# Kernel optimization log

Measured on AMD Instinct MI355X. Metric: run time of the kernel, lower is better.

The kernel has to match this reference:

```python
import jax, jax.numpy as jnp
import numpy as np
import math

B, T, D = 2, 2048, 2048
H, KV, HD = 16, 4, 128  # n_heads, n_kv_heads, head_dim
ROPE_BASE = 10000.0


def setup_inputs() -> dict:
    key = jax.random.key(0)
    ks = jax.random.split(key, 5)
    s = 0.02
    return {
        "x": jax.random.normal(ks[0], (B, T, D), dtype=jnp.float32),
        "Wq": jax.random.normal(ks[1], (D, H * HD), dtype=jnp.float32) * s,
        "Wk": jax.random.normal(ks[2], (D, KV * HD), dtype=jnp.float32) * s,
        "Wv": jax.random.normal(ks[3], (D, KV * HD), dtype=jnp.float32) * s,
        "Wo": jax.random.normal(ks[4], (H * HD, D), dtype=jnp.float32) * s,
    }


def _rope_tables(t_len, dtype):
    inv_freq = 1.0 / (ROPE_BASE ** (jnp.arange(0, HD, 2, dtype=jnp.float32) / HD))
    t = jnp.arange(t_len, dtype=jnp.float32)
    freqs = t[:, None] * inv_freq[None, :]  # [T, HD/2]
    return jnp.cos(freqs).astype(dtype), jnp.sin(freqs).astype(dtype)


def _apply_rope(x, cos, sin):
    # x: [B, h, T, HD]; cos/sin: [T, HD/2] broadcast to [1,1,T,HD/2]
    c = cos[None, None, :, :]
    s = sin[None, None, :, :]
    x1, x2 = x[..., ::2], x[..., 1::2]
    rot = jnp.stack([x1 * c - x2 * s, x1 * s + x2 * c], axis=-1)  # interleave back
    return rot.reshape(x.shape)


def reference(x, Wq, Wk, Wv, Wo):
    b, t, d = x.shape
    q = (x @ Wq).reshape(b, t, H, HD).transpose(0, 2, 1, 3)   # [B,H,T,HD]
    k = (x @ Wk).reshape(b, t, KV, HD).transpose(0, 2, 1, 3)  # [B,KV,T,HD]
    v = (x @ Wv).reshape(b, t, KV, HD).transpose(0, 2, 1, 3)

    cos, sin = _rope_tables(t, x.dtype)
    q = _apply_rope(q, cos, sin)
    k = _apply_rope(k, cos, sin)

    rep = H // KV
    k_rep = jnp.repeat(k, rep, axis=1)  # [B,H,T,HD]
    v_rep = jnp.repeat(v, rep, axis=1)

    scale = 1.0 / math.sqrt(HD)
    scores = jnp.einsum("bhqd,bhkd->bhqk", q, k_rep) * scale
    causal = jnp.triu(jnp.ones((t, t), dtype=bool), k=1)
    neg = jnp.finfo(scores.dtype).min
    scores = jnp.where(causal[None, None, :, :], neg, scores)
    attn = jax.nn.softmax(scores, axis=-1)
    out = jnp.einsum("bhqk,bhkd->bhqd", attn, v_rep)
    y = out.transpose(0, 2, 1, 3).reshape(b, t, H * HD) @ Wo
    return y
```

## Files before the change

### kernel.cpp

```cpp
#include <hip/hip_runtime.h>
#include <cstdint>
#include <math.h>

#define T_SEQ 2048
#define BATCH 2
#define NH 16
#define NKV 4
#define HD 128

typedef __attribute__((ext_vector_type(8))) short short8;
typedef __attribute__((ext_vector_type(4))) float f32x4;

__device__ __forceinline__ ushort f2bf(float f) {
  uint32_t u = __builtin_bit_cast(uint32_t, f);
  u += 0x7FFF + ((u >> 16) & 1);
  return (ushort)(u >> 16);
}
__device__ __forceinline__ ushort f2bf_trunc(float f) {
  return (ushort)(__builtin_bit_cast(uint32_t, f) >> 16);
}
__device__ __forceinline__ float bf2f(ushort u) {
  uint32_t v = ((uint32_t)u) << 16;
  return __builtin_bit_cast(float, v);
}
__device__ __forceinline__ void ld16(void* lds, const void* g) {
  __builtin_amdgcn_global_load_lds((const __attribute__((address_space(1))) void*)g,
                                   (__attribute__((address_space(3))) void*)lds,
                                   16, 0, 0);
}

__global__ __launch_bounds__(256) void prep(
    const float* __restrict__ x, ushort* __restrict__ xb,
    const float* __restrict__ Wq, const float* __restrict__ Wk,
    const float* __restrict__ Wv, const float* __restrict__ Wo,
    ushort* __restrict__ wqkvT, ushort* __restrict__ woT) {
  __shared__ float tile[32][33];
  const int bid = blockIdx.x;
  const int tid = threadIdx.x;
  if (bid < 8192) {
    int i = (bid * 256 + tid) * 4;
    float4 v = *(const float4*)&x[i];
    ushort4 o;
    o.x = f2bf(v.x); o.y = f2bf(v.y); o.z = f2bf(v.z); o.w = f2bf(v.w);
    *(ushort4*)&xb[i] = o;
    return;
  }
  const float* in;
  ushort* out;
  int N, lid;
  if (bid < 12288)      { in = Wq; out = wqkvT;                        N = 2048; lid = bid - 8192; }
  else if (bid < 13312) { in = Wk; out = wqkvT + (size_t)2048 * 2048;  N = 512;  lid = bid - 12288; }
  else if (bid < 14336) { in = Wv; out = wqkvT + (size_t)2560 * 2048;  N = 512;  lid = bid - 13312; }
  else                  { in = Wo; out = woT;                          N = 2048; lid = bid - 14336; }
  const int K = 2048;
  const int nb = N / 32;
  const int n0 = (lid % nb) * 32, k0 = (lid / nb) * 32;
  const int r = tid >> 3, c4 = (tid & 7) << 2;
  float4 v = *(const float4*)&in[(size_t)(k0 + r) * N + n0 + c4];
  tile[r][c4 + 0] = v.x; tile[r][c4 + 1] = v.y;
  tile[r][c4 + 2] = v.z; tile[r][c4 + 3] = v.w;
  __syncthreads();
  ushort4 o;
  o.x = f2bf(tile[c4 + 0][r]); o.y = f2bf(tile[c4 + 1][r]);
  o.z = f2bf(tile[c4 + 2][r]); o.w = f2bf(tile[c4 + 3][r]);
  *(ushort4*)&out[(size_t)(n0 + r) * K + k0 + c4] = o;
}

template <typename OutT>
__global__ __launch_bounds__(256) void gemm_bt(const ushort* __restrict__ A,
                                               const ushort* __restrict__ Bt,
                                               OutT* __restrict__ C,
                                               int M, int N, int K) {
  __shared__ __align__(16) ushort As[128 * 32];
  __shared__ __align__(16) ushort Bs[128 * 32];
  const int tid = threadIdx.x;
  const int w = tid >> 6, l = tid & 63;
  const int wr = w >> 1, wc = w & 1;
  const int quad = l >> 4, l15 = l & 15;
  const int bm = blockIdx.y * 128, bn = blockIdx.x * 128;

  f32x4 acc[4][4];
#pragma unroll
  for (int mi = 0; mi < 4; ++mi)
#pragma unroll
    for (int ni = 0; ni < 4; ++ni)
#pragma unroll
      for (int r = 0; r < 4; ++r) acc[mi][ni][r] = 0.f;

  for (int k0 = 0; k0 < K; k0 += 32) {
    __syncthreads();
#pragma unroll
    for (int j = 0; j < 2; ++j) {
      int r0 = w * 32 + j * 16;
      int row = r0 + (l >> 2);
      int gc = (l & 3) ^ ((row >> 1) & 3);
      ld16(&As[r0 * 32], &A[(size_t)(bm + row) * K + k0 + gc * 8]);
      ld16(&Bs[r0 * 32], &Bt[(size_t)(bn + row) * K + k0 + gc * 8]);
    }
    __syncthreads();
    short8 af[4], bf[4];
#pragma unroll
    for (int mi = 0; mi < 4; ++mi) {
      int m = wr * 64 + mi * 16 + l15;
      af[mi] = *(const short8*)&As[m * 32 + (quad ^ ((m >> 1) & 3)) * 8];
    }
#pragma unroll
    for (int ni = 0; ni < 4; ++ni) {
      int n = wc * 64 + ni * 16 + l15;
      bf[ni] = *(const short8*)&Bs[n * 32 + (quad ^ ((n >> 1) & 3)) * 8];
    }
#pragma unroll
    for (int mi = 0; mi < 4; ++mi)
#pragma unroll
      for (int ni = 0; ni < 4; ++ni)
        acc[mi][ni] = __builtin_amdgcn_mfma_f32_16x16x32_bf16(af[mi], bf[ni], acc[mi][ni], 0, 0, 0);
  }
#pragma unroll
  for (int mi = 0; mi < 4; ++mi)
#pragma unroll
    for (int ni = 0; ni < 4; ++ni)
#pragma unroll
      for (int r = 0; r < 4; ++r) {
        int grow = bm + wr * 64 + mi * 16 + quad * 4 + r;
        int gcol = bn + wc * 64 + ni * 16 + l15;
        if constexpr (__is_same(OutT, ushort))
          C[(size_t)grow * N + gcol] = f2bf(acc[mi][ni][r]);
        else
          C[(size_t)grow * N + gcol] = acc[mi][ni][r];
      }
}

template <typename OutT>
__global__ __launch_bounds__(512, 1) void gemm_bt256(const ushort* __restrict__ A,
                                                     const ushort* __restrict__ Bt,
                                                     OutT* __restrict__ C,
                                                     int M, int N, int K) {
  __shared__ __align__(16) ushort As[2][256 * 64];
  __shared__ __align__(16) ushort Bs[2][256 * 64];
  const int tid = threadIdx.x;
  const int w = tid >> 6, l = tid & 63;
  const int wr = w >> 2, wc = w & 3;
  const int quad = l >> 4, l15 = l & 15;
  const int bm = blockIdx.y * 256, bn = blockIdx.x * 256;

  f32x4 acc[8][4];
#pragma unroll
  for (int mi = 0; mi < 8; ++mi)
#pragma unroll
    for (int ni = 0; ni < 4; ++ni)
#pragma unroll
      for (int r = 0; r < 4; ++r) acc[mi][ni][r] = 0.f;

  auto stage_unit = [&](int k0, int buf, int u) {
    const ushort* __restrict__ src = (u < 2) ? A : Bt;
    ushort* dst = (u < 2) ? &As[buf][0] : &Bs[buf][0];
    const int goff = (u < 2) ? bm : bn;
    const int rb = (u & 1) * 128;
#pragma unroll
    for (int j = 0; j < 2; ++j) {
      int r0 = rb + j * 64 + w * 8;
      int row = r0 + (l >> 3);
      int gc = (l & 7) ^ (row & 7);
      ld16(&dst[r0 * 64], &src[(size_t)(goff + row) * K + k0 + gc * 8]);
    }
  };

  short8 af[4][2], bfv[4][2];

#define LOADA8(mh)                                                             \
  _Pragma("unroll") for (int i = 0; i < 4; ++i) {                              \
    int m = wr * 128 + ((mh) * 4 + i) * 16 + l15;                              \
    _Pragma("unroll") for (int ks = 0; ks < 2; ++ks)                           \
      af[i][ks] = *(const short8*)&as[m * 64 + ((ks * 4 + quad) ^ (m & 7)) * 8]; \
  }
#define LOADB4(nf)                                                             \
  {                                                                            \
    int n = wc * 64 + (nf) * 16 + l15;                                         \
    _Pragma("unroll") for (int ks = 0; ks < 2; ++ks)                           \
      bfv[nf][ks] = *(const short8*)&bs[n * 64 + ((ks * 4 + quad) ^ (n & 7)) * 8]; \
  }
#define MFMA16(mh, nh)                                                         \
  __builtin_amdgcn_s_setprio(1);                                               \
  _Pragma("unroll") for (int ks = 0; ks < 2; ++ks)                             \
  _Pragma("unroll") for (int i = 0; i < 4; ++i)                                \
  _Pragma("unroll") for (int j = 0; j < 2; ++j)                                \
    acc[(mh) * 4 + i][(nh) * 2 + j] = __builtin_amdgcn_mfma_f32_16x16x32_bf16( \
        af[i][ks], bfv[(nh) * 2 + j][ks], acc[(mh) * 4 + i][(nh) * 2 + j],     \
        0, 0, 0);                                                              \
  __builtin_amdgcn_s_setprio(0);

  const int NT = K >> 6;
#pragma unroll
  for (int u = 0; u < 4; ++u) stage_unit(0, 0, u);

  for (int kt = 0; kt < NT; ++kt) {
    const int buf = kt & 1;
    const int nk0 = (kt + 1) << 6;
    const bool pre = (kt + 1 < NT);
    const ushort* as = &As[buf][0];
    const ushort* bs = &Bs[buf][0];

    if (pre) {
      stage_unit(nk0, buf ^ 1, 0);
      asm volatile("s_waitcnt vmcnt(2)" ::: "memory");
    } else {
      asm volatile("s_waitcnt vmcnt(0)" ::: "memory");
    }
    asm volatile("s_barrier" ::: "memory");
    LOADA8(0);
    LOADB4(0); LOADB4(1);
    MFMA16(0, 0);
    asm volatile("s_barrier" ::: "memory");

    if (pre) stage_unit(nk0, buf ^ 1, 1);
    LOADB4(2); LOADB4(3);
    MFMA16(0, 1);
    asm volatile("s_barrier" ::: "memory");

    if (pre) stage_unit(nk0, buf ^ 1, 2);
    LOADA8(1);
    MFMA16(1, 1);
    asm volatile("s_barrier" ::: "memory");

    if (pre) stage_unit(nk0, buf ^ 1, 3);
    MFMA16(1, 0);
    asm volatile("s_barrier" ::: "memory");
  }
#undef LOADA8
#undef LOADB4
#undef MFMA16

#pragma unroll
  for (int mi = 0; mi < 8; ++mi)
#pragma unroll
    for (int ni = 0; ni < 4; ++ni)
#pragma unroll
      for (int r = 0; r < 4; ++r) {
        int grow = bm + wr * 128 + mi * 16 + quad * 4 + r;
        int gcol = bn + wc * 64 + ni * 16 + l15;
        if constexpr (__is_same(OutT, ushort))
          C[(size_t)grow * N + gcol] = f2bf(acc[mi][ni][r]);
        else
          C[(size_t)grow * N + gcol] = acc[mi][ni][r];
      }
}

__global__ __launch_bounds__(256) void rope_k_bf16(ushort* __restrict__ qkv) {
  int idx = blockIdx.x * 256 + threadIdx.x;
  const int PAIRS_PER_ROW = 256;
  if (idx >= BATCH * T_SEQ * PAIRS_PER_ROW) return;
  int row = idx >> 8;
  int kp = idx & 255;
  int t = row & (T_SEQ - 1);
  int i = kp & 63;
  ushort* ptr = qkv + (size_t)row * 3072 + 2048 + 2 * kp;
  float inv = expf((float)i * -0.14391156831212788f);
  float ang = (float)t * inv;
  float sn, cs;
  sincosf(ang, &sn, &cs);
  float x1 = bf2f(ptr[0]), x2 = bf2f(ptr[1]);
  ptr[0] = f2bf(x1 * cs - x2 * sn);
  ptr[1] = f2bf(x1 * sn + x2 * cs);
}

__global__ __launch_bounds__(256) void transpose_v(const ushort* __restrict__ qkv,
                                                   ushort* __restrict__ vT) {
  __shared__ ushort tile[32][34];
  int m0 = blockIdx.x * 32, d0 = blockIdx.y * 32;
  int r = threadIdx.x >> 3, c4 = (threadIdx.x & 7) << 2;
  ushort4 v = *(const ushort4*)&qkv[(size_t)(m0 + r) * 3072 + 2560 + d0 + c4];
  tile[r][c4 + 0] = v.x; tile[r][c4 + 1] = v.y;
  tile[r][c4 + 2] = v.z; tile[r][c4 + 3] = v.w;
  __syncthreads();
  ushort4 o;
  o.x = tile[c4 + 0][r]; o.y = tile[c4 + 1][r];
  o.z = tile[c4 + 2][r]; o.w = tile[c4 + 3][r];
  *(ushort4*)&vT[(size_t)(d0 + r) * 4096 + m0 + c4] = o;
}

__global__ __launch_bounds__(512, 2) void attn_mfma(const ushort* __restrict__ qkv,
                                                    const ushort* __restrict__ vT,
                                                    ushort* __restrict__ ao) {
  __shared__ __align__(16) ushort Ks[2][64 * 128];
  __shared__ __align__(16) ushort Vt[2][128 * 64];
  __shared__ __align__(16) ushort Ps[8][16 * 64];
  const int tid = threadIdx.x;
  const int w = tid >> 6, l = tid & 63;
  const int quad = l >> 4, l15 = l & 15;
  const int hw = w >> 1, sub = w & 1;
  const int kvh = blockIdx.y, b = blockIdx.z;
  const int h = kvh * 4 + hw;
  const size_t krow0 = (size_t)b * T_SEQ;
  const float SC = 0.12751744595764253f;

  ushort* pw = Ps[w];
  const int within = l & 7;
  const int colbase = l15 >> 3;

  auto stage = [&](int kt, int bufi) {
    const int kt0 = kt << 6;
    ushort* kb = Ks[bufi];
    ushort* vb = Vt[bufi];
#pragma unroll
    for (int j = 0; j < 2; ++j) {
      int r0 = w * 8 + j * 4;
      int row = r0 + (l >> 4);
      int gc = (l & 15) ^ ((row >> 1) & 7);
      ld16(&kb[r0 * 128], &qkv[(krow0 + kt0 + row) * 3072 + 2048 + kvh * 128 + gc * 8]);
    }
#pragma unroll
    for (int j = 0; j < 2; ++j) {
      int r0 = w * 16 + j * 8;
      int row = r0 + (l >> 3);
      int gc = (l & 7) ^ (row & 7);
      ld16(&vb[r0 * 64], &vT[(size_t)(kvh * 128 + row) * 4096 + krow0 + kt0 + gc * 8]);
    }
  };

#pragma unroll 1
  for (int ph = 0; ph < 2; ++ph) {
    const int qt = ph ? (int)blockIdx.x : 63 - (int)blockIdx.x;
    const int qt0 = qt << 5;
    const size_t qrow0 = krow0 + qt0;

    const int t_pos = qt0 + sub * 16 + l15;
    short8 qf[4];
#pragma unroll
    for (int kc = 0; kc < 4; ++kc) {
      short8 raw = *(const short8*)&qkv[(qrow0 + sub * 16 + l15) * 3072 + h * 128 + kc * 32 + quad * 8];
#pragma unroll
      for (int u = 0; u < 4; ++u) {
        int i_idx = kc * 16 + quad * 4 + u;
        float inv = expf((float)i_idx * -0.14391156831212788f);
        float sn, cs;
        sincosf((float)t_pos * inv, &sn, &cs);
        cs *= SC; sn *= SC;
        float x1 = bf2f((ushort)raw[2 * u]);
        float x2 = bf2f((ushort)raw[2 * u + 1]);
        qf[kc][2 * u]     = (short)f2bf(x1 * cs - x2 * sn);
        qf[kc][2 * u + 1] = (short)f2bf(x1 * sn + x2 * cs);
      }
    }

    f32x4 oacc[8];
#pragma unroll
    for (int i = 0; i < 8; ++i)
#pragma unroll
      for (int r = 0; r < 4; ++r) oacc[i][r] = 0.f;
    float lpart[4] = {0.f, 0.f, 0.f, 0.f};

    const int nkt = (qt >> 1) + 1;
    __syncthreads();
    stage(0, 0);
    for (int kt = 0; kt < nkt; ++kt) {
      __syncthreads();
      if (kt + 1 < nkt) stage(kt + 1, (kt + 1) & 1);
      const ushort* kb = Ks[kt & 1];
      const ushort* vb = Vt[kt & 1];

      f32x4 sacc[4];
#pragma unroll
      for (int ni = 0; ni < 4; ++ni)
#pragma unroll
        for (int r = 0; r < 4; ++r) sacc[ni][r] = 0.f;
#pragma unroll
      for (int kc = 0; kc < 4; ++kc) {
#pragma unroll
        for (int ni = 0; ni < 4; ++ni) {
          int n = ni * 16 + l15;
          short8 bfr = *(const short8*)&kb[n * 128 + ((kc * 4 + quad) ^ ((n >> 1) & 7)) * 8];
          sacc[ni] = __builtin_amdgcn_mfma_f32_16x16x32_bf16(qf[kc], bfr, sacc[ni], 0, 0, 0);
        }
      }

      const int kt0 = kt << 6;
      if (kt == nkt - 1) {
        const int rowg = qt0 + sub * 16 + quad * 4;
#pragma unroll
        for (int ni = 0; ni < 4; ++ni) {
          const int colid = kt0 + ni * 16 + l15;
#pragma unroll
          for (int r = 0; r < 4; ++r) {
            float s = (colid > rowg + r) ? -1e30f : sacc[ni][r];
            float pv = __builtin_amdgcn_exp2f(s);
            lpart[r] += pv;
            int prow = quad * 4 + r;
            pw[prow * 64 + (((ni * 2 + colbase) ^ (prow & 7)) << 3) + within] = f2bf_trunc(pv);
          }
        }
      } else {
#pragma unroll
        for (int ni = 0; ni < 4; ++ni)
#pragma unroll
          for (int r = 0; r < 4; ++r) {
            float pv = __builtin_amdgcn_exp2f(sacc[ni][r]);
            lpart[r] += pv;
            int prow = quad * 4 + r;
            pw[prow * 64 + (((ni * 2 + colbase) ^ (prow & 7)) << 3) + within] = f2bf_trunc(pv);
          }
      }

#pragma unroll
      for (int kc = 0; kc < 2; ++kc) {
        short8 a = *(const short8*)&pw[l15 * 64 + ((kc * 4 + quad) ^ (l15 & 7)) * 8];
#pragma unroll
        for (int ni2 = 0; ni2 < 8; ++ni2) {
          int d = ni2 * 16 + l15;
          short8 bfr = *(const short8*)&vb[d * 64 + ((kc * 4 + quad) ^ (d & 7)) * 8];
          oacc[ni2] = __builtin_amdgcn_mfma_f32_16x16x32_bf16(a, bfr, oacc[ni2], 0, 0, 0);
        }
      }
    }

#pragma unroll
    for (int r = 0; r < 4; ++r) {
      float lv = lpart[r];
      lv += __shfl_xor(lv, 1);
      lv += __shfl_xor(lv, 2);
      lv += __shfl_xor(lv, 4);
      lv += __shfl_xor(lv, 8);
      float inv = 1.f / lv;
      size_t grow = qrow0 + sub * 16 + quad * 4 + r;
#pragma unroll
      for (int ni2 = 0; ni2 < 8; ++ni2)
        ao[grow * 2048 + h * 128 + ni2 * 16 + l15] = f2bf(oacc[ni2][r] * inv);
    }
  }
}

extern "C" void kernel_launch(void* const* d_in, const int* in_sizes, int n_in,
                              void* d_out, int out_size, void* d_ws, size_t ws_size,
                              hipStream_t stream) {
  const float* x  = (const float*)d_in[0];
  const float* Wq = (const float*)d_in[1];
  const float* Wk = (const float*)d_in[2];
  const float* Wv = (const float*)d_in[3];
  const float* Wo = (const float*)d_in[4];
  float* y = (float*)d_out;

  const int M = BATCH * T_SEQ;
  ushort* xb    = (ushort*)d_ws;
  ushort* wqkvT = xb + (size_t)M * 2048;
  ushort* woT   = wqkvT + (size_t)3072 * 2048;
  ushort* qkv   = woT + (size_t)2048 * 2048;
  ushort* vTb   = qkv + (size_t)M * 3072;
  ushort* aob   = vTb + (size_t)512 * 4096;

  prep<<<18432, 256, 0, stream>>>(x, xb, Wq, Wk, Wv, Wo, wqkvT, woT);

  gemm_bt256<ushort><<<dim3(3072 / 256, M / 256), 512, 0, stream>>>(
      xb, wqkvT, qkv, M, 3072, 2048);

  rope_k_bf16<<<(M * 256 + 255) / 256, 256, 0, stream>>>(qkv);
  transpose_v<<<dim3(M / 32, 512 / 32), 256, 0, stream>>>(qkv, vTb);

  attn_mfma<<<dim3(32, NKV, BATCH), 512, 0, stream>>>(qkv, vTb, aob);

  gemm_bt<float><<<dim3(2048 / 128, M / 128), 256, 0, stream>>>(
      aob, woT, y, M, 2048, 2048);
}
```

Baseline: 319.7 us.

## Deepen GEMM prefetch pipeline, remap workgroups per XCD, raise occupancy bound

Restructures the 256x256 bf16 GEMM main loop so A-tile units for step k+2 are issued into the current buffer after its A fragments are in registers. Separate lo/hi fragment registers replace the single A/B fragment arrays, and the wait counts change to match. It also remaps workgroup IDs into 8 contiguous chunks, presumably to improve L2 locality across XCDs, and changes launch_bounds to request 2 blocks per CU. The risks are register spilling from the occupancy hint and subtle hazards in the reordered barrier/waitcnt scheme. The remap also assumes the grid size is divisible by 8.

Result: no change. 321.4 us (+0.5%).

```diff
diff --git a/kernel.cpp b/kernel.cpp
--- a/kernel.cpp
+++ b/kernel.cpp
@@ -131,7 +131,7 @@
 }
 
 template <typename OutT>
-__global__ __launch_bounds__(512, 1) void gemm_bt256(const ushort* __restrict__ A,
+__global__ __launch_bounds__(512, 2) void gemm_bt256(const ushort* __restrict__ A,
                                                      const ushort* __restrict__ Bt,
                                                      OutT* __restrict__ C,
                                                      int M, int N, int K) {
@@ -141,7 +141,12 @@
   const int w = tid >> 6, l = tid & 63;
   const int wr = w >> 2, wc = w & 3;
   const int quad = l >> 4, l15 = l & 15;
-  const int bm = blockIdx.y * 256, bn = blockIdx.x * 256;
+
+  const int nwg = gridDim.x * gridDim.y;
+  int lin = blockIdx.y * gridDim.x + blockIdx.x;
+  const int cpx = nwg >> 3;
+  lin = (lin & 7) * cpx + (lin >> 3);
+  const int bm = (lin / gridDim.x) * 256, bn = (lin % gridDim.x) * 256;
 
   f32x4 acc[8][4];
 #pragma unroll
@@ -165,70 +170,70 @@
     }
   };
 
-  short8 af[4][2], bfv[4][2];
-
-#define LOADA8(mh)                                                             \
-  _Pragma("unroll") for (int i = 0; i < 4; ++i) {                              \
-    int m = wr * 128 + ((mh) * 4 + i) * 16 + l15;                              \
-    _Pragma("unroll") for (int ks = 0; ks < 2; ++ks)                           \
-      af[i][ks] = *(const short8*)&as[m * 64 + ((ks * 4 + quad) ^ (m & 7)) * 8]; \
-  }
-#define LOADB4(nf)                                                             \
-  {                                                                            \
-    int n = wc * 64 + (nf) * 16 + l15;                                         \
-    _Pragma("unroll") for (int ks = 0; ks < 2; ++ks)                           \
-      bfv[nf][ks] = *(const short8*)&bs[n * 64 + ((ks * 4 + quad) ^ (n & 7)) * 8]; \
-  }
-#define MFMA16(mh, nh)                                                         \
-  __builtin_amdgcn_s_setprio(1);                                               \
-  _Pragma("unroll") for (int ks = 0; ks < 2; ++ks)                             \
-  _Pragma("unroll") for (int i = 0; i < 4; ++i)                                \
-  _Pragma("unroll") for (int j = 0; j < 2; ++j)                                \
-    acc[(mh) * 4 + i][(nh) * 2 + j] = __builtin_amdgcn_mfma_f32_16x16x32_bf16( \
-        af[i][ks], bfv[(nh) * 2 + j][ks], acc[(mh) * 4 + i][(nh) * 2 + j],     \
-        0, 0, 0);                                                              \
+  short8 alo[4][2], ahi[4][2], blo[2][2], bhi[2][2];
+
+#define LOAD_A(dst, mh)                                                          \
+  _Pragma("unroll") for (int i = 0; i < 4; ++i) {                                \
+    int m = wr * 128 + ((mh) * 4 + i) * 16 + l15;                                \
+    _Pragma("unroll") for (int ks = 0; ks < 2; ++ks)                             \
+      dst[i][ks] = *(const short8*)&as[m * 64 + ((ks * 4 + quad) ^ (m & 7)) * 8]; \
+  }
+#define LOAD_B(dst, nh)                                                          \
+  _Pragma("unroll") for (int jn = 0; jn < 2; ++jn) {                             \
+    int n = wc * 64 + ((nh) * 2 + jn) * 16 + l15;                                \
+    _Pragma("unroll") for (int ks = 0; ks < 2; ++ks)                             \
+      dst[jn][ks] = *(const short8*)&bs[n * 64 + ((ks * 4 + quad) ^ (n & 7)) * 8]; \
+  }
+#define MFMA_Q(afr, mh, bfr, nh)                                                 \
+  __builtin_amdgcn_s_setprio(1);                                                 \
+  _Pragma("unroll") for (int ks = 0; ks < 2; ++ks)                               \
+  _Pragma("unroll") for (int i = 0; i < 4; ++i)                                  \
+  _Pragma("unroll") for (int jn = 0; jn < 2; ++jn)                               \
+    acc[(mh) * 4 + i][(nh) * 2 + jn] = __builtin_amdgcn_mfma_f32_16x16x32_bf16(  \
+        afr[i][ks], bfr[jn][ks], acc[(mh) * 4 + i][(nh) * 2 + jn], 0, 0, 0);     \
   __builtin_amdgcn_s_setprio(0);
 
   const int NT = K >> 6;
-#pragma unroll
-  for (int u = 0; u < 4; ++u) stage_unit(0, 0, u);
+  stage_unit(0, 0, 0); stage_unit(0, 0, 1);
+  stage_unit(0, 0, 2); stage_unit(0, 0, 3);
+  stage_unit(64, 1, 0); stage_unit(64, 1, 1);
 
   for (int kt = 0; kt < NT; ++kt) {
     const int buf = kt & 1;
-    const int nk0 = (kt + 1) << 6;
-    const bool pre = (kt + 1 < NT);
     const ushort* as = &As[buf][0];
     const ushort* bs = &Bs[buf][0];
-
-    if (pre) {
-      stage_unit(nk0, buf ^ 1, 0);
-      asm volatile("s_waitcnt vmcnt(2)" ::: "memory");
+    const int n1 = (kt + 1) << 6, n2 = (kt + 2) << 6;
+
+    if (kt + 1 < NT) {
+      stage_unit(n1, buf ^ 1, 2);
+      asm volatile("s_waitcnt vmcnt(6)" ::: "memory");
     } else {
       asm volatile("s_waitcnt vmcnt(0)" ::: "memory");
     }
     asm volatile("s_barrier" ::: "memory");
-    LOADA8(0);
-    LOADB4(0); LOADB4(1);
-    MFMA16(0, 0);
-    asm volatile("s_barrier" ::: "memory");
-
-    if (pre) stage_unit(nk0, buf ^ 1, 1);
-    LOADB4(2); LOADB4(3);
-    MFMA16(0, 1);
-    asm volatile("s_barrier" ::: "memory");
-
-    if (pre) stage_unit(nk0, buf ^ 1, 2);
-    LOADA8(1);
-    MFMA16(1, 1);
-    asm volatile("s_barrier" ::: "memory");
-
-    if (pre) stage_unit(nk0, buf ^ 1, 3);
-    MFMA16(1, 0);
-    asm volatile("s_barrier" ::: "memory");
-  }
-#undef LOADA8
-#undef LOADB4
-#undef MFMA16
+    LOAD_A(alo, 0);
+    LOAD_B(blo, 0);
+    MFMA_Q(alo, 0, blo, 0);
+    asm volatile("s_barrier" ::: "memory");
+
+    if (kt + 1 < NT) stage_unit(n1, buf ^ 1, 3);
+    LOAD_A(ahi, 1);
+    asm volatile("s_barrier" ::: "memory");
+    MFMA_Q(ahi, 1, blo, 0);
+    asm volatile("s_barrier" ::: "memory");
+
+    if (kt + 2 < NT) stage_unit(n2, buf, 0);
+    LOAD_B(bhi, 1);
+    asm volatile("s_barrier" ::: "memory");
+    MFMA_Q(ahi, 1, bhi, 1);
+    asm volatile("s_barrier" ::: "memory");
+
+    if (kt + 2 < NT) stage_unit(n2, buf, 1);
+    MFMA_Q(alo, 0, bhi, 1);
+  }
+#undef LOAD_A
+#undef LOAD_B
+#undef MFMA_Q
 
 #pragma unroll
   for (int mi = 0; mi < 8; ++mi)
```
